# Performance work log

Measured on AMD Instinct MI355X. Metric: run time of the kernel, lower is better.

Reference implementation:

```python
import jax, jax.numpy as jnp
import numpy as np

D_MODEL = 1024
H = 16
D_K = D_MODEL // H
SEQ = 4096
SIM_WEIGHT = 1.0


def setup_inputs() -> dict:
    key = jax.random.key(0)
    ks = jax.random.split(key, 10)
    s = 1.0 / np.sqrt(D_MODEL)
    return {
        "x": jax.random.normal(ks[0], (SEQ, D_MODEL), dtype=jnp.float32),
        "similarity_matrix": jax.random.normal(ks[1], (SEQ, SEQ), dtype=jnp.float32),
        "w_q": jax.random.normal(ks[2], (D_MODEL, D_MODEL), dtype=jnp.float32) * s,
        "b_q": jnp.zeros((D_MODEL,), dtype=jnp.float32),
        "w_k": jax.random.normal(ks[3], (D_MODEL, D_MODEL), dtype=jnp.float32) * s,
        "b_k": jnp.zeros((D_MODEL,), dtype=jnp.float32),
        "w_v": jax.random.normal(ks[4], (D_MODEL, D_MODEL), dtype=jnp.float32) * s,
        "b_v": jnp.zeros((D_MODEL,), dtype=jnp.float32),
        "w_o": jax.random.normal(ks[5], (D_MODEL, D_MODEL), dtype=jnp.float32) * s,
        "b_o": jnp.zeros((D_MODEL,), dtype=jnp.float32),
    }


def reference(x, similarity_matrix, w_q, b_q, w_k, b_k, w_v, b_v, w_o, b_o):
    # x: [S, D]; project and split heads -> [H, S, d_k]
    q = (x @ w_q.T + b_q).reshape(SEQ, H, D_K).transpose(1, 0, 2)
    k = (x @ w_k.T + b_k).reshape(SEQ, H, D_K).transpose(1, 0, 2)
    v = (x @ w_v.T + b_v).reshape(SEQ, H, D_K).transpose(1, 0, 2)
    # scores: [H, S, S]; additive similarity bias broadcast over heads
    scores = jnp.einsum("hsd,htd->hst", q, k) / jnp.sqrt(jnp.float32(D_K))
    scores = scores + similarity_matrix[None, :, :] * SIM_WEIGHT
    attn = jax.nn.softmax(scores, axis=-1)
    out = jnp.einsum("hst,htd->hsd", attn, v)  # [H, S, d_k]
    out = out.transpose(1, 0, 2).reshape(SEQ, D_MODEL)
    return out @ w_o.T + b_o
```

## Files before the change

kernel.cpp:

```cpp
#include <hip/hip_runtime.h>
#include <hip/hip_bf16.h>

typedef __hip_bfloat16 bf16;
typedef __attribute__((ext_vector_type(8))) short short8;
typedef __attribute__((ext_vector_type(4))) float f32x4;

#define SEQ    4096
#define DMODEL 1024
#define NHEAD  16
#define DKH    64

#define LSTRIDE 72
#define SSTRIDE 68
#define GSTRIDE 40

__device__ __forceinline__ float ldf(const float* p, size_t i) { return p[i]; }
__device__ __forceinline__ float ldf(const bf16*  p, size_t i) { return __bfloat162float(p[i]); }
__device__ __forceinline__ void stf(float* p, size_t i, float v) { p[i] = v; }
__device__ __forceinline__ void stf(bf16*  p, size_t i, float v) { p[i] = __float2bfloat16(v); }

__device__ __forceinline__ short f2bs(float v) {
    bf16 b = __float2bfloat16(v);
    return *(short*)&b;
}
__device__ __forceinline__ float bs2f(short s) {
    bf16 b; *(short*)&b = s;
    return __bfloat162float(b);
}

__device__ __forceinline__ short8 lda8(const bf16* p, size_t i) {
    return *(const short8*)(p + i);
}
__device__ __forceinline__ short8 lda8(const float* p, size_t i) {
    float4 a = *(const float4*)(p + i);
    float4 b = *(const float4*)(p + i + 4);
    short8 r;
    r[0] = f2bs(a.x); r[1] = f2bs(a.y); r[2] = f2bs(a.z); r[3] = f2bs(a.w);
    r[4] = f2bs(b.x); r[5] = f2bs(b.y); r[6] = f2bs(b.z); r[7] = f2bs(b.w);
    return r;
}

__global__ void detect_dtype(const unsigned short* __restrict__ x, int* __restrict__ flag) {
    int lane = threadIdx.x;
    int cnt = 0;
    for (int i = lane; i < 512; i += 64) {
        int e = (x[i] >> 7) & 0xFF;
        cnt += (e >= 100 && e <= 140) ? 1 : 0;
    }
    #pragma unroll
    for (int off = 32; off; off >>= 1) cnt += __shfl_xor(cnt, off, 64);
    if (lane == 0) *flag = (cnt >= 400) ? 1 : 0;
}

template <typename TA, typename TB, typename TC>
__device__ void gemm_mfma_body(const TA* __restrict__ A, const TB* __restrict__ B,
                               const TB* __restrict__ bias, TC* __restrict__ C,
                               int M, int N, int K, short* As, short* Bs) {
    const int tid = threadIdx.x;
    const int w = tid >> 6, lane = tid & 63, q = lane >> 4, c = lane & 15;
    const int m0 = blockIdx.x * 128, n0 = blockIdx.y * 128;
    const int mb = 64 * (w & 1), nb = 64 * (w >> 1);

    f32x4 acc[4][4] = {};

    for (int k0 = 0; k0 < K; k0 += 32) {
        __syncthreads();
        #pragma unroll
        for (int i = 0; i < 2; ++i) {
            int ch = tid + 256 * i;
            int r = ch >> 2, c8 = (ch & 3) * 8;
            *(short8*)&As[r * GSTRIDE + c8] = lda8(A, (size_t)(m0 + r) * K + k0 + c8);
            *(short8*)&Bs[r * GSTRIDE + c8] = lda8(B, (size_t)(n0 + r) * K + k0 + c8);
        }
        __syncthreads();
        short8 af[4], bfr[4];
        #pragma unroll
        for (int i = 0; i < 4; ++i)
            af[i] = *(const short8*)&As[(mb + i * 16 + c) * GSTRIDE + q * 8];
        #pragma unroll
        for (int j = 0; j < 4; ++j)
            bfr[j] = *(const short8*)&Bs[(nb + j * 16 + c) * GSTRIDE + q * 8];
        #pragma unroll
        for (int i = 0; i < 4; ++i)
            #pragma unroll
            for (int j = 0; j < 4; ++j)
                acc[i][j] = __builtin_amdgcn_mfma_f32_16x16x32_bf16(af[i], bfr[j], acc[i][j], 0, 0, 0);
    }

    #pragma unroll
    for (int j = 0; j < 4; ++j) {
        int n = n0 + nb + j * 16 + c;
        float bj = ldf(bias, (size_t)n);
        #pragma unroll
        for (int i = 0; i < 4; ++i)
            #pragma unroll
            for (int t = 0; t < 4; ++t) {
                int m = m0 + mb + i * 16 + q * 4 + t;
                stf(C, (size_t)m * N + n, acc[i][j][t] + bj);
            }
    }
}

__global__ __launch_bounds__(256)
void gemm_proj_mfma(const void* __restrict__ A, const void* __restrict__ B,
                    const void* __restrict__ bias, bf16* __restrict__ C,
                    const int* __restrict__ flag, int M, int N, int K) {
    __shared__ __align__(16) short As[128 * GSTRIDE];
    __shared__ __align__(16) short Bs[128 * GSTRIDE];
    if (*flag)
        gemm_mfma_body<bf16, bf16, bf16>((const bf16*)A, (const bf16*)B, (const bf16*)bias, C, M, N, K, As, Bs);
    else
        gemm_mfma_body<float, float, bf16>((const float*)A, (const float*)B, (const float*)bias, C, M, N, K, As, Bs);
}

__global__ __launch_bounds__(256)
void gemm_out_mfma(const bf16* __restrict__ A, const void* __restrict__ B,
                   const void* __restrict__ bias, void* __restrict__ C,
                   const int* __restrict__ flag, int M, int N, int K) {
    __shared__ __align__(16) short As[128 * GSTRIDE];
    __shared__ __align__(16) short Bs[128 * GSTRIDE];
    if (*flag)
        gemm_mfma_body<bf16, bf16, bf16>(A, (const bf16*)B, (const bf16*)bias, (bf16*)C, M, N, K, As, Bs);
    else
        gemm_mfma_body<bf16, float, float>(A, (const float*)B, (const float*)bias, (float*)C, M, N, K, As, Bs);
}

__global__ __launch_bounds__(256)
void flash_mfma(const bf16* __restrict__ Q, const bf16* __restrict__ Kg,
                const bf16* __restrict__ Vg, const void* __restrict__ simv,
                bf16* __restrict__ O, const int* __restrict__ flag) {
    __shared__ __align__(16) short Qs[64 * LSTRIDE];
    __shared__ __align__(16) short Ks[64 * LSTRIDE];
    __shared__ __align__(16) short Vt[64 * LSTRIDE];
    __shared__ __align__(16) short Ps[64 * LSTRIDE];
    __shared__ __align__(16) float Ss[64 * SSTRIDE];

    const int tid = threadIdx.x;
    const int w = tid >> 6, lane = tid & 63, q = lane >> 4, c = lane & 15;
    const int q0 = blockIdx.x * 64, hd = blockIdx.y * DKH;
    const bool isbf = (*flag != 0);
    const bf16* simb = (const bf16*)simv;
    const float* simf = (const float*)simv;

    #pragma unroll
    for (int i = 0; i < 2; ++i) {
        int ch = tid + 256 * i;
        int r = ch >> 3, c8 = (ch & 7) * 8;
        *(short8*)&Qs[r * LSTRIDE + c8] = *(const short8*)&Q[(size_t)(q0 + r) * DMODEL + hd + c8];
    }

    f32x4 accO[4] = {};
    float Mrow[4], Lrow[4];
    #pragma unroll
    for (int i = 0; i < 4; ++i) { Mrow[i] = -1e30f; Lrow[i] = 0.f; }

    for (int t = 0; t < SEQ / 64; ++t) {
        const int k0 = t * 64;
        __syncthreads();

        #pragma unroll
        for (int i = 0; i < 2; ++i) {
            int ch = tid + 256 * i;
            int r = ch >> 3, c8 = (ch & 7) * 8;
            *(short8*)&Ks[r * LSTRIDE + c8] = *(const short8*)&Kg[(size_t)(k0 + r) * DMODEL + hd + c8];
        }
        #pragma unroll
        for (int i = 0; i < 2; ++i) {
            int d = tid & 63, n0 = ((tid >> 6) + 4 * i) * 8;
            short8 vv;
            #pragma unroll
            for (int j = 0; j < 8; ++j) {
                bf16 b = Vg[(size_t)(k0 + n0 + j) * DMODEL + hd + d];
                vv[j] = *(short*)&b;
            }
            *(short8*)&Vt[d * LSTRIDE + n0] = vv;
        }
        if (isbf) {
            #pragma unroll
            for (int i = 0; i < 2; ++i) {
                int ch = tid + 256 * i;
                int r = ch >> 3, c8 = (ch & 7) * 8;
                short8 sv8 = *(const short8*)&simb[(size_t)(q0 + r) * SEQ + k0 + c8];
                float4 lo, hi;
                lo.x = bs2f(sv8[0]); lo.y = bs2f(sv8[1]); lo.z = bs2f(sv8[2]); lo.w = bs2f(sv8[3]);
                hi.x = bs2f(sv8[4]); hi.y = bs2f(sv8[5]); hi.z = bs2f(sv8[6]); hi.w = bs2f(sv8[7]);
                *(float4*)&Ss[r * SSTRIDE + c8] = lo;
                *(float4*)&Ss[r * SSTRIDE + c8 + 4] = hi;
            }
        } else {
            #pragma unroll
            for (int i = 0; i < 4; ++i) {
                int ch = tid + 256 * i;
                int r = ch >> 4, c4 = (ch & 15) * 4;
                *(float4*)&Ss[r * SSTRIDE + c4] = *(const float4*)&simf[(size_t)(q0 + r) * SEQ + k0 + c4];
            }
        }
        __syncthreads();

        short8 aq0 = *(const short8*)&Qs[(16 * w + c) * LSTRIDE + q * 8];
        short8 aq1 = *(const short8*)&Qs[(16 * w + c) * LSTRIDE + 32 + q * 8];
        f32x4 sfr[4];
        #pragma unroll
        for (int f = 0; f < 4; ++f) {
            short8 bk0 = *(const short8*)&Ks[(f * 16 + c) * LSTRIDE + q * 8];
            short8 bk1 = *(const short8*)&Ks[(f * 16 + c) * LSTRIDE + 32 + q * 8];
            f32x4 a = {};
            a = __builtin_amdgcn_mfma_f32_16x16x32_bf16(aq0, bk0, a, 0, 0, 0);
            a = __builtin_amdgcn_mfma_f32_16x16x32_bf16(aq1, bk1, a, 0, 0, 0);
            sfr[f] = a;
        }

        float sv[4][4], rmax[4];
        #pragma unroll
        for (int i = 0; i < 4; ++i) rmax[i] = -1e30f;
        #pragma unroll
        for (int f = 0; f < 4; ++f)
            #pragma unroll
            for (int i = 0; i < 4; ++i) {
                float s = sfr[f][i] * 0.125f + Ss[(16 * w + q * 4 + i) * SSTRIDE + f * 16 + c];
                sv[f][i] = s;
                rmax[i] = fmaxf(rmax[i], s);
            }
        #pragma unroll
        for (int off = 1; off < 16; off <<= 1)
            #pragma unroll
            for (int i = 0; i < 4; ++i)
                rmax[i] = fmaxf(rmax[i], __shfl_xor(rmax[i], off, 64));

        float alpha[4], rsum[4];
        #pragma unroll
        for (int i = 0; i < 4; ++i) {
            float mn = fmaxf(Mrow[i], rmax[i]);
            alpha[i] = __expf(Mrow[i] - mn);
            Mrow[i] = mn;
            rsum[i] = 0.f;
        }
        #pragma unroll
        for (int f = 0; f < 4; ++f)
            #pragma unroll
            for (int i = 0; i < 4; ++i) {
                float p = __expf(sv[f][i] - Mrow[i]);
                sv[f][i] = p;
                rsum[i] += p;
            }
        #pragma unroll
        for (int off = 1; off < 16; off <<= 1)
            #pragma unroll
            for (int i = 0; i < 4; ++i)
                rsum[i] += __shfl_xor(rsum[i], off, 64);
        #pragma unroll
        for (int i = 0; i < 4; ++i)
            Lrow[i] = Lrow[i] * alpha[i] + rsum[i];

        #pragma unroll
        for (int f = 0; f < 4; ++f)
            #pragma unroll
            for (int i = 0; i < 4; ++i)
                Ps[(16 * w + q * 4 + i) * LSTRIDE + f * 16 + c] = f2bs(sv[f][i]);

        #pragma unroll
        for (int f = 0; f < 4; ++f)
            #pragma unroll
            for (int i = 0; i < 4; ++i)
                accO[f][i] *= alpha[i];

        __syncthreads();

        short8 ap0 = *(const short8*)&Ps[(16 * w + c) * LSTRIDE + q * 8];
        short8 ap1 = *(const short8*)&Ps[(16 * w + c) * LSTRIDE + 32 + q * 8];
        #pragma unroll
        for (int f = 0; f < 4; ++f) {
            short8 bv0 = *(const short8*)&Vt[(f * 16 + c) * LSTRIDE + q * 8];
            short8 bv1 = *(const short8*)&Vt[(f * 16 + c) * LSTRIDE + 32 + q * 8];
            accO[f] = __builtin_amdgcn_mfma_f32_16x16x32_bf16(ap0, bv0, accO[f], 0, 0, 0);
            accO[f] = __builtin_amdgcn_mfma_f32_16x16x32_bf16(ap1, bv1, accO[f], 0, 0, 0);
        }
    }

    #pragma unroll
    for (int i = 0; i < 4; ++i) {
        float inv = 1.f / Lrow[i];
        int gr = q0 + 16 * w + q * 4 + i;
        #pragma unroll
        for (int f = 0; f < 4; ++f)
            O[(size_t)gr * DMODEL + hd + f * 16 + c] = __float2bfloat16(accO[f][i] * inv);
    }
}

extern "C" void kernel_launch(void* const* d_in, const int* in_sizes, int n_in,
                              void* d_out, int out_size, void* d_ws, size_t ws_size,
                              hipStream_t stream) {
    int* flagw = (int*)d_ws;
    const int* flag = (const int*)d_ws;
    bf16* Q = (bf16*)((char*)d_ws + 256);
    bf16* K = Q + (size_t)SEQ * DMODEL;
    bf16* V = K + (size_t)SEQ * DMODEL;
    bf16* O = V + (size_t)SEQ * DMODEL;

    detect_dtype<<<1, 64, 0, stream>>>((const unsigned short*)d_in[0], flagw);

    dim3 gg(SEQ / 128, DMODEL / 128);
    dim3 blk(256);
    gemm_proj_mfma<<<gg, blk, 0, stream>>>(d_in[0], d_in[2], d_in[3], Q, flag, SEQ, DMODEL, DMODEL);
    gemm_proj_mfma<<<gg, blk, 0, stream>>>(d_in[0], d_in[4], d_in[5], K, flag, SEQ, DMODEL, DMODEL);
    gemm_proj_mfma<<<gg, blk, 0, stream>>>(d_in[0], d_in[6], d_in[7], V, flag, SEQ, DMODEL, DMODEL);

    flash_mfma<<<dim3(SEQ / 64, NHEAD), blk, 0, stream>>>(Q, K, V, d_in[1], O, flag);

    gemm_out_mfma<<<gg, blk, 0, stream>>>(O, d_in[8], d_in[9], d_out, flag, SEQ, DMODEL, DMODEL);
}
```

Baseline: 615.3 us.

## Write V transposed from projection, load sim bias directly to registers, widen GEMM K-tile

```diff
diff --git a/kernel.cpp b/kernel.cpp
--- a/kernel.cpp
+++ b/kernel.cpp
@@ -11,8 +11,7 @@
 #define DKH    64
 
 #define LSTRIDE 72
-#define SSTRIDE 68
-#define GSTRIDE 40
+#define KSTRIDE 72
 
 __device__ __forceinline__ float ldf(const float* p, size_t i) { return p[i]; }
 __device__ __forceinline__ float ldf(const bf16*  p, size_t i) { return __bfloat162float(p[i]); }
@@ -22,10 +21,6 @@
 __device__ __forceinline__ short f2bs(float v) {
     bf16 b = __float2bfloat16(v);
     return *(short*)&b;
-}
-__device__ __forceinline__ float bs2f(short s) {
-    bf16 b; *(short*)&b = s;
-    return __bfloat162float(b);
 }
 
 __device__ __forceinline__ short8 lda8(const bf16* p, size_t i) {
@@ -52,7 +47,7 @@
     if (lane == 0) *flag = (cnt >= 400) ? 1 : 0;
 }
 
-template <typename TA, typename TB, typename TC>
+template <typename TA, typename TB, typename TC, bool TRANSC>
 __device__ void gemm_mfma_body(const TA* __restrict__ A, const TB* __restrict__ B,
                                const TB* __restrict__ bias, TC* __restrict__ C,
                                int M, int N, int K, short* As, short* Bs) {
@@ -63,28 +58,32 @@
 
     f32x4 acc[4][4] = {};
 
-    for (int k0 = 0; k0 < K; k0 += 32) {
+    for (int k0 = 0; k0 < K; k0 += 64) {
         __syncthreads();
         #pragma unroll
-        for (int i = 0; i < 2; ++i) {
+        for (int i = 0; i < 4; ++i) {
             int ch = tid + 256 * i;
-            int r = ch >> 2, c8 = (ch & 3) * 8;
-            *(short8*)&As[r * GSTRIDE + c8] = lda8(A, (size_t)(m0 + r) * K + k0 + c8);
-            *(short8*)&Bs[r * GSTRIDE + c8] = lda8(B, (size_t)(n0 + r) * K + k0 + c8);
+            int r = ch >> 3, c8 = (ch & 7) * 8;
+            *(short8*)&As[r * KSTRIDE + c8] = lda8(A, (size_t)(m0 + r) * K + k0 + c8);
+            *(short8*)&Bs[r * KSTRIDE + c8] = lda8(B, (size_t)(n0 + r) * K + k0 + c8);
         }
         __syncthreads();
-        short8 af[4], bfr[4];
-        #pragma unroll
-        for (int i = 0; i < 4; ++i)
-            af[i] = *(const short8*)&As[(mb + i * 16 + c) * GSTRIDE + q * 8];
-        #pragma unroll
-        for (int j = 0; j < 4; ++j)
-            bfr[j] = *(const short8*)&Bs[(nb + j * 16 + c) * GSTRIDE + q * 8];
-        #pragma unroll
-        for (int i = 0; i < 4; ++i)
+        #pragma unroll
+        for (int kh = 0; kh < 2; ++kh) {
+            const int kk = kh * 32 + q * 8;
+            short8 af[4], bfr[4];
+            #pragma unroll
+            for (int i = 0; i < 4; ++i)
+                af[i] = *(const short8*)&As[(mb + i * 16 + c) * KSTRIDE + kk];
             #pragma unroll
             for (int j = 0; j < 4; ++j)
-                acc[i][j] = __builtin_amdgcn_mfma_f32_16x16x32_bf16(af[i], bfr[j], acc[i][j], 0, 0, 0);
+                bfr[j] = *(const short8*)&Bs[(nb + j * 16 + c) * KSTRIDE + kk];
+            #pragma unroll
+            for (int i = 0; i < 4; ++i)
+                #pragma unroll
+                for (int j = 0; j < 4; ++j)
+                    acc[i][j] = __builtin_amdgcn_mfma_f32_16x16x32_bf16(af[i], bfr[j], acc[i][j], 0, 0, 0);
+        }
     }
 
     #pragma unroll
@@ -92,12 +91,23 @@
         int n = n0 + nb + j * 16 + c;
         float bj = ldf(bias, (size_t)n);
         #pragma unroll
-        for (int i = 0; i < 4; ++i)
-            #pragma unroll
-            for (int t = 0; t < 4; ++t) {
-                int m = m0 + mb + i * 16 + q * 4 + t;
-                stf(C, (size_t)m * N + n, acc[i][j][t] + bj);
+        for (int i = 0; i < 4; ++i) {
+            if (TRANSC) {
+                short4 pk;
+                pk.x = f2bs(acc[i][j][0] + bj);
+                pk.y = f2bs(acc[i][j][1] + bj);
+                pk.z = f2bs(acc[i][j][2] + bj);
+                pk.w = f2bs(acc[i][j][3] + bj);
+                int m = m0 + mb + i * 16 + q * 4;
+                *(short4*)&((bf16*)C)[(size_t)n * M + m] = pk;
+            } else {
+                #pragma unroll
+                for (int t = 0; t < 4; ++t) {
+                    int m = m0 + mb + i * 16 + q * 4 + t;
+                    stf(C, (size_t)m * N + n, acc[i][j][t] + bj);
+                }
             }
+        }
     }
 }
 
@@ -105,42 +115,46 @@
 void gemm_proj_mfma(const void* __restrict__ A, const void* __restrict__ B,
                     const void* __restrict__ bias, bf16* __restrict__ C,
                     const int* __restrict__ flag, int M, int N, int K) {
-    __shared__ __align__(16) short As[128 * GSTRIDE];
-    __shared__ __align__(16) short Bs[128 * GSTRIDE];
+    __shared__ __align__(16) short As[128 * KSTRIDE];
+    __shared__ __align__(16) short Bs[128 * KSTRIDE];
     if (*flag)
-        gemm_mfma_body<bf16, bf16, bf16>((const bf16*)A, (const bf16*)B, (const bf16*)bias, C, M, N, K, As, Bs);
+        gemm_mfma_body<bf16, bf16, bf16, false>((const bf16*)A, (const bf16*)B, (const bf16*)bias, C, M, N, K, As, Bs);
     else
-        gemm_mfma_body<float, float, bf16>((const float*)A, (const float*)B, (const float*)bias, C, M, N, K, As, Bs);
+        gemm_mfma_body<float, float, bf16, false>((const float*)A, (const float*)B, (const float*)bias, C, M, N, K, As, Bs);
+}
+
+__global__ __launch_bounds__(256)
+void gemm_projT_mfma(const void* __restrict__ A, const void* __restrict__ B,
+                     const void* __restrict__ bias, bf16* __restrict__ C,
+                     const int* __restrict__ flag, int M, int N, int K) {
+    __shared__ __align__(16) short As[128 * KSTRIDE];
+    __shared__ __align__(16) short Bs[128 * KSTRIDE];
+    if (*flag)
+        gemm_mfma_body<bf16, bf16, bf16, true>((const bf16*)A, (const bf16*)B, (const bf16*)bias, C, M, N, K, As, Bs);
+    else
+        gemm_mfma_body<float, float, bf16, true>((const float*)A, (const float*)B, (const float*)bias, C, M, N, K, As, Bs);
 }
 
 __global__ __launch_bounds__(256)
 void gemm_out_mfma(const bf16* __restrict__ A, const void* __restrict__ B,
                    const void* __restrict__ bias, void* __restrict__ C,
                    const int* __restrict__ flag, int M, int N, int K) {
-    __shared__ __align__(16) short As[128 * GSTRIDE];
-    __shared__ __align__(16) short Bs[128 * GSTRIDE];
+    __shared__ __align__(16) short As[128 * KSTRIDE];
+    __shared__ __align__(16) short Bs[128 * KSTRIDE];
     if (*flag)
-        gemm_mfma_body<bf16, bf16, bf16>(A, (const bf16*)B, (const bf16*)bias, (bf16*)C, M, N, K, As, Bs);
+        gemm_mfma_body<bf16, bf16, bf16, false>(A, (const bf16*)B, (const bf16*)bias, (bf16*)C, M, N, K, As, Bs);
     else
-        gemm_mfma_body<bf16, float, float>(A, (const float*)B, (const float*)bias, (float*)C, M, N, K, As, Bs);
-}
-
-__global__ __launch_bounds__(256)
-void flash_mfma(const bf16* __restrict__ Q, const bf16* __restrict__ Kg,
-                const bf16* __restrict__ Vg, const void* __restrict__ simv,
-                bf16* __restrict__ O, const int* __restrict__ flag) {
-    __shared__ __align__(16) short Qs[64 * LSTRIDE];
-    __shared__ __align__(16) short Ks[64 * LSTRIDE];
-    __shared__ __align__(16) short Vt[64 * LSTRIDE];
-    __shared__ __align__(16) short Ps[64 * LSTRIDE];
-    __shared__ __align__(16) float Ss[64 * SSTRIDE];
-
+        gemm_mfma_body<bf16, float, float, false>(A, (const float*)B, (const float*)bias, (float*)C, M, N, K, As, Bs);
+}
+
+template <typename TS>
+__device__ void flash_body(const bf16* __restrict__ Q, const bf16* __restrict__ Kg,
+                           const bf16* __restrict__ VtG, const TS* __restrict__ sim,
+                           bf16* __restrict__ O,
+                           short* Qs, short* Ks, short* Vt, short* Ps) {
     const int tid = threadIdx.x;
     const int w = tid >> 6, lane = tid & 63, q = lane >> 4, c = lane & 15;
     const int q0 = blockIdx.x * 64, hd = blockIdx.y * DKH;
-    const bool isbf = (*flag != 0);
-    const bf16* simb = (const bf16*)simv;
-    const float* simf = (const float*)simv;
 
     #pragma unroll
     for (int i = 0; i < 2; ++i) {
@@ -163,39 +177,16 @@
             int ch = tid + 256 * i;
             int r = ch >> 3, c8 = (ch & 7) * 8;
             *(short8*)&Ks[r * LSTRIDE + c8] = *(const short8*)&Kg[(size_t)(k0 + r) * DMODEL + hd + c8];
-        }
-        #pragma unroll
-        for (int i = 0; i < 2; ++i) {
-            int d = tid & 63, n0 = ((tid >> 6) + 4 * i) * 8;
-            short8 vv;
-            #pragma unroll
-            for (int j = 0; j < 8; ++j) {
-                bf16 b = Vg[(size_t)(k0 + n0 + j) * DMODEL + hd + d];
-                vv[j] = *(short*)&b;
-            }
-            *(short8*)&Vt[d * LSTRIDE + n0] = vv;
-        }
-        if (isbf) {
-            #pragma unroll
-            for (int i = 0; i < 2; ++i) {
-                int ch = tid + 256 * i;
-                int r = ch >> 3, c8 = (ch & 7) * 8;
-                short8 sv8 = *(const short8*)&simb[(size_t)(q0 + r) * SEQ + k0 + c8];
-                float4 lo, hi;
-                lo.x = bs2f(sv8[0]); lo.y = bs2f(sv8[1]); lo.z = bs2f(sv8[2]); lo.w = bs2f(sv8[3]);
-                hi.x = bs2f(sv8[4]); hi.y = bs2f(sv8[5]); hi.z = bs2f(sv8[6]); hi.w = bs2f(sv8[7]);
-                *(float4*)&Ss[r * SSTRIDE + c8] = lo;
-                *(float4*)&Ss[r * SSTRIDE + c8 + 4] = hi;
-            }
-        } else {
-            #pragma unroll
-            for (int i = 0; i < 4; ++i) {
-                int ch = tid + 256 * i;
-                int r = ch >> 4, c4 = (ch & 15) * 4;
-                *(float4*)&Ss[r * SSTRIDE + c4] = *(const float4*)&simf[(size_t)(q0 + r) * SEQ + k0 + c4];
-            }
+            *(short8*)&Vt[r * LSTRIDE + c8] = *(const short8*)&VtG[(size_t)(hd + r) * SEQ + k0 + c8];
         }
         __syncthreads();
+
+        float sm[4][4];
+        #pragma unroll
+        for (int f = 0; f < 4; ++f)
+            #pragma unroll
+            for (int i = 0; i < 4; ++i)
+                sm[f][i] = ldf(sim, (size_t)(q0 + 16 * w + q * 4 + i) * SEQ + k0 + f * 16 + c);
 
         short8 aq0 = *(const short8*)&Qs[(16 * w + c) * LSTRIDE + q * 8];
         short8 aq1 = *(const short8*)&Qs[(16 * w + c) * LSTRIDE + 32 + q * 8];
@@ -217,7 +208,7 @@
         for (int f = 0; f < 4; ++f)
             #pragma unroll
             for (int i = 0; i < 4; ++i) {
-                float s = sfr[f][i] * 0.125f + Ss[(16 * w + q * 4 + i) * SSTRIDE + f * 16 + c];
+                float s = sfr[f][i] * 0.125f + sm[f][i];
                 sv[f][i] = s;
                 rmax[i] = fmaxf(rmax[i], s);
             }
@@ -264,8 +255,6 @@
             for (int i = 0; i < 4; ++i)
                 accO[f][i] *= alpha[i];
 
-        __syncthreads();
-
         short8 ap0 = *(const short8*)&Ps[(16 * w + c) * LSTRIDE + q * 8];
         short8 ap1 = *(const short8*)&Ps[(16 * w + c) * LSTRIDE + 32 + q * 8];
         #pragma unroll
@@ -287,25 +276,39 @@
     }
 }
 
+__global__ __launch_bounds__(256)
+void flash_mfma(const bf16* __restrict__ Q, const bf16* __restrict__ K,
+                const bf16* __restrict__ Vt, const void* __restrict__ sim,
+                bf16* __restrict__ O, const int* __restrict__ flag) {
+    __shared__ __align__(16) short Qs[64 * LSTRIDE];
+    __shared__ __align__(16) short Ks[64 * LSTRIDE];
+    __shared__ __align__(16) short Vs[64 * LSTRIDE];
+    __shared__ __align__(16) short Ps[64 * LSTRIDE];
+    if (*flag)
+        flash_body<bf16>(Q, K, Vt, (const bf16*)sim, O, Qs, Ks, Vs, Ps);
+    else
+        flash_body<float>(Q, K, Vt, (const float*)sim, O, Qs, Ks, Vs, Ps);
+}
+
 extern "C" void kernel_launch(void* const* d_in, const int* in_sizes, int n_in,
                               void* d_out, int out_size, void* d_ws, size_t ws_size,
                               hipStream_t stream) {
     int* flagw = (int*)d_ws;
     const int* flag = (const int*)d_ws;
-    bf16* Q = (bf16*)((char*)d_ws + 256);
-    bf16* K = Q + (size_t)SEQ * DMODEL;
-    bf16* V = K + (size_t)SEQ * DMODEL;
-    bf16* O = V + (size_t)SEQ * DMODEL;
+    bf16* Q  = (bf16*)((char*)d_ws + 256);
+    bf16* K  = Q + (size_t)SEQ * DMODEL;
+    bf16* Vt = K + (size_t)SEQ * DMODEL;
+    bf16* O  = Vt + (size_t)SEQ * DMODEL;
 
     detect_dtype<<<1, 64, 0, stream>>>((const unsigned short*)d_in[0], flagw);
 
     dim3 gg(SEQ / 128, DMODEL / 128);
     dim3 blk(256);
-    gemm_proj_mfma<<<gg, blk, 0, stream>>>(d_in[0], d_in[2], d_in[3], Q, flag, SEQ, DMODEL, DMODEL);
-    gemm_proj_mfma<<<gg, blk, 0, stream>>>(d_in[0], d_in[4], d_in[5], K, flag, SEQ, DMODEL, DMODEL);
-    gemm_proj_mfma<<<gg, blk, 0, stream>>>(d_in[0], d_in[6], d_in[7], V, flag, SEQ, DMODEL, DMODEL);
-
-    flash_mfma<<<dim3(SEQ / 64, NHEAD), blk, 0, stream>>>(Q, K, V, d_in[1], O, flag);
+    gemm_proj_mfma <<<gg, blk, 0, stream>>>(d_in[0], d_in[2], d_in[3], Q,  flag, SEQ, DMODEL, DMODEL);
+    gemm_proj_mfma <<<gg, blk, 0, stream>>>(d_in[0], d_in[4], d_in[5], K,  flag, SEQ, DMODEL, DMODEL);
+    gemm_projT_mfma<<<gg, blk, 0, stream>>>(d_in[0], d_in[6], d_in[7], Vt, flag, SEQ, DMODEL, DMODEL);
+
+    flash_mfma<<<dim3(SEQ / 64, NHEAD), blk, 0, stream>>>(Q, K, Vt, d_in[1], O, flag);
 
     gemm_out_mfma<<<gg, blk, 0, stream>>>(O, d_in[8], d_in[9], d_out, flag, SEQ, DMODEL, DMODEL);
 }
```

New measurement: 518.8 us. 1.19x faster.
